# Kernel tuning notes

Hardware: AMD Instinct MI355X
Metric: run time of the kernel (lower is better)

Reference implementation:

```python
import jax, jax.numpy as jnp
import numpy as np

N = 50000      # num_nodes
NT = 300000    # unique (s, o) pairs
R = 64         # num relations
RP = 16        # latent pseudo-relations
E = 32         # emb_dim
C = 32         # num_classes
LW = 64        # latent MLP width


def setup_inputs() -> dict:
    key = jax.random.key(0)
    ks = jax.random.split(key, 12)
    inp = {
        "s_idx": jax.random.randint(ks[0], (NT,), 0, N, dtype=jnp.int32),
        "o_idx": jax.random.randint(ks[1], (NT,), 0, N, dtype=jnp.int32),
        "nhots": jax.random.uniform(ks[2], (NT, R), dtype=jnp.float32),
        "W1a": jax.random.normal(ks[3], (R, LW), dtype=jnp.float32) * 0.1,
        "b1a": jnp.zeros((LW,), jnp.float32),
        "W1b": jax.random.normal(ks[4], (LW, RP), dtype=jnp.float32) * 0.1,
        "b1b": jnp.zeros((RP,), jnp.float32),
        "W2a": jax.random.normal(ks[5], (R, LW), dtype=jnp.float32) * 0.1,
        "b2a": jnp.zeros((LW,), jnp.float32),
        "W2b": jax.random.normal(ks[6], (LW, RP), dtype=jnp.float32) * 0.1,
        "b2b": jnp.zeros((RP,), jnp.float32),
        "weights1": jax.random.normal(ks[7], (RP, N, E), dtype=jnp.float32) * 0.05,
        "weights2": jax.random.normal(ks[8], (RP, E, C), dtype=jnp.float32) * 0.05,
        "bias1": jnp.zeros((E,), jnp.float32),
        "bias2": jnp.zeros((C,), jnp.float32),
    }
    return inp


def _mlp(x, Wa, ba, Wb, bb):
    # Linear(r, lwidth) -> ReLU -> Linear(lwidth, rp)
    return jax.nn.relu(x @ Wa + ba) @ Wb + bb


def reference(s_idx, o_idx, nhots, W1a, b1a, W1b, b1b, W2a, b2a, W2b, b2b,
              weights1, weights2, bias1, bias2):
    n, rp = N, RP
    e = weights1.shape[2]
    k = jnp.arange(rp, dtype=s_idx.dtype)[:, None]   # [rp, 1]

    # hindices: rows = s (tiled k-major), cols = o * k  -> sparse (n, n*rp)
    hrows = jnp.tile(s_idx, rp)                       # [rp*nt]
    hcols = (o_idx[None, :] * k).reshape(-1)          # [rp*nt]
    # vindices: rows = s * k, cols = o (tiled)        -> sparse (n*rp, n)
    vrows = (s_idx[None, :] * k).reshape(-1)
    vcols = jnp.tile(o_idx, rp)

    # ---- layer 1: latent relation softmax + column-normalized spmm ----
    lat1 = jax.nn.softmax(_mlp(nhots, W1a, b1a, W1b, b1b), axis=1)  # [nt, rp]
    v1 = lat1.T.reshape(-1)                                          # [rp*nt], k-major
    colsum = jax.ops.segment_sum(v1, hcols, num_segments=n * rp)
    v1 = v1 / colsum[hcols]
    # spmm: out[s] += v1 * weights1.view(rp*n, e)[o*k]
    h = jax.ops.segment_sum(v1[:, None] * weights1.reshape(rp * n, e)[hcols],
                            hrows, num_segments=n)                   # [n, e]
    h = jax.nn.relu(h + bias1)

    # ---- layer 2: latent relation softmax + row-normalized spmm ----
    lat2 = jax.nn.softmax(_mlp(nhots, W2a, b2a, W2b, b2b), axis=1)   # [nt, rp]
    v2 = lat2.T.reshape(-1)
    rowsum = jax.ops.segment_sum(v2, vrows, num_segments=n * rp)
    v2 = v2 / rowsum[vrows]
    # spmm: out[s*k] += v2 * h[o]
    h2 = jax.ops.segment_sum(v2[:, None] * h[vcols],
                             vrows, num_segments=n * rp)             # [n*rp, e]
    h2 = h2.reshape(rp, n, e)

    out = jnp.einsum('rhc,rnh->nc', weights2, h2) + bias2            # [n, c]
    return out
```

## Files before the change

### kernel.cpp

```cpp
#include <hip/hip_runtime.h>
#include <hip/hip_bf16.h>

#define DEV_INLINE __device__ __forceinline__

constexpr int kN   = 50000;
constexpr int kNT  = 300000;
constexpr int kR   = 64;
constexpr int kRP  = 16;
constexpr int kE   = 32;
constexpr int kC   = 32;
constexpr int kLW  = 64;
constexpr int kNRP = kN * kRP;
constexpr int kChunks = (kN + 255) / 256;

typedef __attribute__((ext_vector_type(8))) short s8v;
typedef __attribute__((ext_vector_type(4))) float f32x4;

DEV_INLINE short f2bf(float f) {
  union { float f; unsigned u; } v; v.f = f;
  unsigned r = (v.u + 0x7fffu + ((v.u >> 16) & 1u)) >> 16;
  return (short)r;
}
DEV_INLINE float bf2f(short s) {
  union { unsigned u; float f; } v; v.u = ((unsigned)(unsigned short)s) << 16;
  return v.f;
}
DEV_INLINE float bflo(unsigned u) { union { unsigned x; float f; } a; a.x = u << 16;        return a.f; }
DEV_INLINE float bfhi(unsigned u) { union { unsigned x; float f; } a; a.x = u & 0xffff0000u; return a.f; }

union U4S8 { uint4 u; s8v s; };

DEV_INLINE void split8(const float4 A, const float4 B, s8v& hi, s8v& lo) {
  const float f[8] = {A.x, A.y, A.z, A.w, B.x, B.y, B.z, B.w};
  unsigned u[8], l[8];
#pragma unroll
  for (int i = 0; i < 8; i++) { union { float f; unsigned u; } c; c.f = f[i]; u[i] = c.u; }
#pragma unroll
  for (int i = 0; i < 8; i++) {
    union { unsigned u; float f; } t; t.u = u[i] & 0xffff0000u;
    union { float f; unsigned u; } c; c.f = f[i] - t.f; l[i] = c.u;
  }
  U4S8 H, L;
  H.u.x = (u[1] & 0xffff0000u) | (u[0] >> 16);
  H.u.y = (u[3] & 0xffff0000u) | (u[2] >> 16);
  H.u.z = (u[5] & 0xffff0000u) | (u[4] >> 16);
  H.u.w = (u[7] & 0xffff0000u) | (u[6] >> 16);
  L.u.x = (l[1] & 0xffff0000u) | (l[0] >> 16);
  L.u.y = (l[3] & 0xffff0000u) | (l[2] >> 16);
  L.u.z = (l[5] & 0xffff0000u) | (l[4] >> 16);
  L.u.w = (l[7] & 0xffff0000u) | (l[6] >> 16);
  hi = H.s; lo = L.s;
}

__global__ void __launch_bounds__(256)
k_count(const int* __restrict__ s_idx, const int* __restrict__ o_idx,
        int* __restrict__ cnt_s, int* __restrict__ cnt_o) {
  const int e = blockIdx.x * 256 + threadIdx.x;
  if (e < kNT) {
    atomicAdd(&cnt_s[s_idx[e]], 1);
    atomicAdd(&cnt_o[o_idx[e]], 1);
  }
}

__global__ void __launch_bounds__(256)
k_scan_p1(const int* __restrict__ cnt_s, const int* __restrict__ cnt_o,
          int* __restrict__ rp_s, int* __restrict__ rp_o,
          int* __restrict__ bs_s, int* __restrict__ bs_o) {
  const int b = blockIdx.x;
  const bool iso = b >= kChunks;
  const int chunk = iso ? b - kChunks : b;
  const int* cnt = iso ? cnt_o : cnt_s;
  int* rp = iso ? rp_o : rp_s;
  int* bs = iso ? bs_o : bs_s;
  __shared__ int ws[4];
  const int tid = threadIdx.x, wave = tid >> 6, lane = tid & 63;
  const int i = chunk * 256 + tid;
  int v = (i < kN) ? cnt[i] : 0;
  int incl = v;
#pragma unroll
  for (int off = 1; off < 64; off <<= 1) {
    int tmp = __shfl_up(incl, off, 64);
    if (lane >= off) incl += tmp;
  }
  if (lane == 63) ws[wave] = incl;
  __syncthreads();
  int add = 0;
#pragma unroll
  for (int w = 0; w < 4; w++) if (w < wave) add += ws[w];
  incl += add;
  if (i < kN) rp[i + 1] = incl;
  if (tid == 255) bs[chunk] = incl;
}

__global__ void __launch_bounds__(256)
k_scan_p2(int* __restrict__ bs_s, int* __restrict__ bs_o) {
  __shared__ int ws[4];
  const int tid = threadIdx.x, wave = tid >> 6, lane = tid & 63;
#pragma unroll 1
  for (int a = 0; a < 2; a++) {
    int* bs = a ? bs_o : bs_s;
    const int v = (tid < kChunks) ? bs[tid] : 0;
    int incl = v;
#pragma unroll
    for (int off = 1; off < 64; off <<= 1) {
      int tmp = __shfl_up(incl, off, 64);
      if (lane >= off) incl += tmp;
    }
    if (lane == 63) ws[wave] = incl;
    __syncthreads();
    int add = 0;
#pragma unroll
    for (int w = 0; w < 4; w++) if (w < wave) add += ws[w];
    incl += add;
    __syncthreads();
    if (tid < kChunks) bs[tid] = incl - v;
    __syncthreads();
  }
}

__global__ void __launch_bounds__(256)
k_scan_p3(const int* __restrict__ bs_s, const int* __restrict__ bs_o,
          int* __restrict__ rp_s, int* __restrict__ rp_o) {
  const int b = blockIdx.x;
  const bool iso = b >= kChunks;
  const int chunk = iso ? b - kChunks : b;
  int* rp = iso ? rp_o : rp_s;
  const int* bs = iso ? bs_o : bs_s;
  const int i = chunk * 256 + threadIdx.x;
  if (i < kN) rp[i + 1] += bs[chunk];
  if (chunk == 0 && threadIdx.x == 0) rp[0] = 0;
}

__global__ void __launch_bounds__(256)
k_scatter2(const int* __restrict__ s_idx, const int* __restrict__ o_idx,
           const int* __restrict__ rowptr_s, int* __restrict__ cursor_s,
           const int* __restrict__ rowptr_o, int* __restrict__ cursor_o,
           int2* __restrict__ eo_s, int* __restrict__ e_o) {
  const int e = blockIdx.x * 256 + threadIdx.x;
  if (e < kNT) {
    const int s = s_idx[e], o = o_idx[e];
    const int ps = atomicAdd(&cursor_s[s], 1);
    int2 v; v.x = e; v.y = o;
    eo_s[rowptr_s[s] + ps] = v;
    const int po = atomicAdd(&cursor_o[o], 1);
    e_o[rowptr_o[o] + po] = e;
  }
}

__global__ void __launch_bounds__(256)
k_wprep(const float* __restrict__ W1a, const float* __restrict__ W1b,
        const float* __restrict__ W2a, const float* __restrict__ W2b,
        short* __restrict__ Wf) {
  const int tid = threadIdx.x;
  for (int i = tid; i < 8192; i += 256) {
    const int j = i & 7, lane = (i >> 3) & 63, ks = (i >> 9) & 1,
              nt = (i >> 10) & 3, mlp = i >> 12;
    const int p = lane & 15, q8 = (lane >> 4) * 8;
    const float* Wa = mlp ? W2a : W1a;
    const float v = Wa[(ks * 32 + q8 + j) * kLW + nt * 16 + p];
    union { float f; unsigned u; } c; c.f = v;
    const short h = (short)(c.u >> 16);
    Wf[i] = h;
    Wf[8192 + i] = f2bf(v - bf2f(h));
  }
  for (int i = tid; i < 2048; i += 256) {
    const int j = i & 7, lane = (i >> 3) & 63, ks = (i >> 9) & 1, mlp = i >> 10;
    const int p = lane & 15, q8 = (lane >> 4) * 8;
    const float* Wb = mlp ? W2b : W1b;
    const float v = Wb[(ks * 32 + q8 + j) * kRP + p];
    union { float f; unsigned u; } c; c.f = v;
    const short h = (short)(c.u >> 16);
    Wf[16384 + i] = h;
    Wf[18432 + i] = f2bf(v - bf2f(h));
  }
}

__global__ void __launch_bounds__(256)
k_lat(const float* __restrict__ nhots, const short* __restrict__ Wf,
      const float* __restrict__ b1a, const float* __restrict__ b1b,
      const float* __restrict__ b2a, const float* __restrict__ b2b,
      float* __restrict__ lat1o, float* __restrict__ lat2o) {
  __shared__ float sHf[4][16][68];
  const int tid = threadIdx.x;
  const int wave = tid >> 6, lane = tid & 63;
  const int p = lane & 15, q = lane >> 4, q8 = (lane >> 4) * 8;

  const uint4* BaH4 = (const uint4*)(Wf);
  const uint4* BaL4 = (const uint4*)(Wf + 8192);
  const uint4* BbH4 = (const uint4*)(Wf + 16384);
  const uint4* BbL4 = (const uint4*)(Wf + 18432);

  const int w2 = (blockIdx.x * 4 + wave) * 2;

#pragma unroll 1
  for (int mlp = 0; mlp < 2; mlp++) {
    s8v Bh[4][2], Bl[4][2], Bbh[2], Bbl[2];
#pragma unroll
    for (int nt = 0; nt < 4; nt++)
#pragma unroll
      for (int ks = 0; ks < 2; ks++) {
        U4S8 a, b;
        a.u = BaH4[((mlp * 4 + nt) * 2 + ks) * 64 + lane];
        b.u = BaL4[((mlp * 4 + nt) * 2 + ks) * 64 + lane];
        Bh[nt][ks] = a.s; Bl[nt][ks] = b.s;
      }
#pragma unroll
    for (int ks = 0; ks < 2; ks++) {
      U4S8 a, b;
      a.u = BbH4[(mlp * 2 + ks) * 64 + lane];
      b.u = BbL4[(mlp * 2 + ks) * 64 + lane];
      Bbh[ks] = a.s; Bbl[ks] = b.s;
    }
    const float* bA = mlp ? b2a : b1a;
    const float* bB = mlp ? b2b : b1b;
    float bav[4];
#pragma unroll
    for (int nt = 0; nt < 4; nt++) bav[nt] = bA[nt * 16 + p];
    const float bbv = bB[p];
    float* lato = mlp ? lat2o : lat1o;

#pragma unroll 1
    for (int t = 0; t < 2; t++) {
      const int slot = w2 + t;
      if (slot >= kNT / 32) break;
      const int eb = slot * 32;
#pragma unroll 1
      for (int ht = 0; ht < 2; ht++) {
        const int mb = eb + ht * 16;
        const float* arow = nhots + (size_t)(mb + p) * kR;
        s8v ah[2], al[2];
#pragma unroll
        for (int ks = 0; ks < 2; ks++) {
          const float4 xa = *(const float4*)(arow + ks * 32 + q8);
          const float4 xb = *(const float4*)(arow + ks * 32 + q8 + 4);
          split8(xa, xb, ah[ks], al[ks]);
        }
        f32x4 acc[4];
#pragma unroll
        for (int nt = 0; nt < 4; nt++) {
          acc[nt] = (f32x4)0.f;
#pragma unroll
          for (int ks = 0; ks < 2; ks++) {
            acc[nt] = __builtin_amdgcn_mfma_f32_16x16x32_bf16(ah[ks], Bh[nt][ks], acc[nt], 0, 0, 0);
            acc[nt] = __builtin_amdgcn_mfma_f32_16x16x32_bf16(ah[ks], Bl[nt][ks], acc[nt], 0, 0, 0);
            acc[nt] = __builtin_amdgcn_mfma_f32_16x16x32_bf16(al[ks], Bh[nt][ks], acc[nt], 0, 0, 0);
          }
        }
#pragma unroll
        for (int nt = 0; nt < 4; nt++)
#pragma unroll
          for (int reg = 0; reg < 4; reg++)
            sHf[wave][q * 4 + reg][nt * 16 + p] = fmaxf(acc[nt][reg] + bav[nt], 0.f);
        const float* hr = &sHf[wave][p][0];
        s8v hh[2], hl[2];
#pragma unroll
        for (int ks = 0; ks < 2; ks++) {
          const float4 xa = *(const float4*)(hr + ks * 32 + q8);
          const float4 xb = *(const float4*)(hr + ks * 32 + q8 + 4);
          split8(xa, xb, hh[ks], hl[ks]);
        }
        f32x4 accB = (f32x4)0.f;
#pragma unroll
        for (int ks = 0; ks < 2; ks++) {
          accB = __builtin_amdgcn_mfma_f32_16x16x32_bf16(hh[ks], Bbh[ks], accB, 0, 0, 0);
          accB = __builtin_amdgcn_mfma_f32_16x16x32_bf16(hh[ks], Bbl[ks], accB, 0, 0, 0);
          accB = __builtin_amdgcn_mfma_f32_16x16x32_bf16(hl[ks], Bbh[ks], accB, 0, 0, 0);
        }
#pragma unroll
        for (int reg = 0; reg < 4; reg++) {
          const float v = accB[reg] + bbv;
          float m = v;
#pragma unroll
          for (int d = 1; d < 16; d <<= 1) m = fmaxf(m, __shfl_xor(m, d));
          const float e = __expf(v - m);
          float sum = e;
#pragma unroll
          for (int d = 1; d < 16; d <<= 1) sum += __shfl_xor(sum, d);
          lato[(size_t)(mb + q * 4 + reg) * kRP + p] = e / sum;
        }
      }
    }
  }
}

__global__ void __launch_bounds__(256)
k_partials(const int* __restrict__ rowptr_s, const int2* __restrict__ eo_s,
           const int* __restrict__ rowptr_o, const int* __restrict__ e_o,
           const float* __restrict__ lat1, const float* __restrict__ lat2,
           float* __restrict__ C1, float* __restrict__ R2,
           float* __restrict__ tots) {
  __shared__ float st[2][4];
  const int tid = threadIdx.x;
  const int wave = tid >> 6, lane = tid & 63;
  const int k = lane & 15, g = lane >> 4;
  float t1 = 0.f, t2 = 0.f;
  const int nw = gridDim.x * 4;
  for (int n = blockIdx.x * 4 + wave; n < kN; n += nw) {
    {
      const int beg = rowptr_s[n], end = rowptr_s[n + 1];
      float acc = 0.f;
      for (int j = beg + g; j < end; j += 4)
        acc += lat2[(size_t)eo_s[j].x * kRP + k];
      acc += __shfl_xor(acc, 16); acc += __shfl_xor(acc, 32);
      if (g == 0) { R2[n * kRP + k] = acc; if (k == 0) t2 += acc; }
    }
    {
      const int beg = rowptr_o[n], end = rowptr_o[n + 1];
      float acc = 0.f;
      for (int j = beg + g; j < end; j += 4)
        acc += lat1[(size_t)e_o[j] * kRP + k];
      acc += __shfl_xor(acc, 16); acc += __shfl_xor(acc, 32);
      if (g == 0) { C1[n * kRP + k] = acc; if (k == 0) t1 += acc; }
    }
  }
  if (lane == 0) { st[0][wave] = t1; st[1][wave] = t2; }
  __syncthreads();
  if (tid == 0) {
    atomicAdd(&tots[0], st[0][0] + st[0][1] + st[0][2] + st[0][3]);
    atomicAdd(&tots[1], st[1][0] + st[1][1] + st[1][2] + st[1][3]);
  }
}

__global__ void __launch_bounds__(256)
k_norms(const float* __restrict__ C1, const float* __restrict__ R2,
        const float* __restrict__ tots,
        float* __restrict__ csinv, float* __restrict__ rsinv) {
  const int m = blockIdx.x * 256 + threadIdx.x;
  if (m < kNRP) {
    float cs = (m == 0) ? tots[0] : 0.f;
    float rs = (m == 0) ? tots[1] : 0.f;
#pragma unroll
    for (int k = 1; k < kRP; k++) {
      if (m % k == 0) {
        const int q = m / k;
        if (q < kN) { cs += C1[q * kRP + k]; rs += R2[q * kRP + k]; }
      }
    }
    csinv[m] = (cs != 0.f) ? 1.f / cs : 0.f;
    rsinv[m] = (rs != 0.f) ? 1.f / rs : 0.f;
  }
}

__global__ void __launch_bounds__(256)
k_gbuild(const float* __restrict__ wt1, const float* __restrict__ csinv,
         unsigned* __restrict__ G8u) {
  __shared__ float sT[16][33];
  const int o = blockIdx.x;
  const int tid = threadIdx.x;
#pragma unroll
  for (int half = 0; half < 2; half++) {
    const int e = half * 256 + tid;
    const int k = e >> 5, c = e & 31;
    const int idx = o * k;
    sT[k][c] = csinv[idx] * wt1[(size_t)idx * kE + c];
  }
  __syncthreads();
  const int l = tid >> 2;
  const int c = l >> 1, kh = l & 1;
  const int j0 = (2 * tid) & 7;
  const int k0 = kh * 8 + j0, k1 = k0 + 1;
  const unsigned lo = (unsigned short)f2bf(sT[k0][c]);
  const unsigned hi = (unsigned short)f2bf(sT[k1][c]);
  G8u[(size_t)o * 256 + tid] = lo | (hi << 16);
}

__global__ void __launch_bounds__(256)
k_layer1g(const int* __restrict__ rowptr, const int2* __restrict__ eo,
          const float* __restrict__ lat1, const uint4* __restrict__ G8,
          const float* __restrict__ bias1, float* __restrict__ h) {
  const int tid = threadIdx.x;
  const int wave = tid >> 6, lane = tid & 63;
  const int c = lane >> 1, kh = lane & 1;
  const float b1 = bias1[c];
  for (int s = blockIdx.x * 4 + wave; s < kN; s += gridDim.x * 4) {
    float acc = 0.f;
    const int beg = rowptr[s], end = rowptr[s + 1];
    for (int j = beg; j < end; j++) {
      const int2 E = eo[j];
      const uint4 g = G8[(size_t)E.y * 64 + lane];
      const float4 la = *(const float4*)(lat1 + (size_t)E.x * kRP + kh * 8);
      const float4 lb = *(const float4*)(lat1 + (size_t)E.x * kRP + kh * 8 + 4);
      acc = fmaf(la.x, bflo(g.x), acc); acc = fmaf(la.y, bfhi(g.x), acc);
      acc = fmaf(la.z, bflo(g.y), acc); acc = fmaf(la.w, bfhi(g.y), acc);
      acc = fmaf(lb.x, bflo(g.z), acc); acc = fmaf(lb.y, bfhi(g.z), acc);
      acc = fmaf(lb.z, bflo(g.w), acc); acc = fmaf(lb.w, bfhi(g.w), acc);
    }
    acc += __shfl_xor(acc, 1);
    if (kh == 0) h[(size_t)s * kE + c] = fmaxf(acc + b1, 0.f);
  }
}

__global__ void __launch_bounds__(256)
k_u(const int* __restrict__ rowptr, const int2* __restrict__ eo,
    const float* __restrict__ lat2, const float* __restrict__ rsinv,
    const float* __restrict__ h, short* __restrict__ Ub,
    float* __restrict__ pblk) {
  __shared__ float sacc[kE];
  const int tid = threadIdx.x;
  const int wave = tid >> 6, lane = tid & 63;
  const int c = lane & 31, half = lane >> 5;
  if (tid < kE) sacc[tid] = 0.f;
  __syncthreads();
  float hpart = 0.f;
  for (int s = blockIdx.x * 4 + wave; s < kN; s += gridDim.x * 4) {
    float u[8];
#pragma unroll
    for (int kk = 0; kk < 8; kk++) u[kk] = 0.f;
    const int beg = rowptr[s], end = rowptr[s + 1];
    for (int j = beg; j < end; j++) {
      const int2 E = eo[j];
      const float hv = h[(size_t)E.y * kE + c];
      const float4* lp = (const float4*)(lat2 + (size_t)E.x * kRP) + half * 2;
      const float4 la = lp[0], lb = lp[1];
      const float lv[8] = {la.x, la.y, la.z, la.w, lb.x, lb.y, lb.z, lb.w};
#pragma unroll
      for (int kk = 0; kk < 8; kk++) u[kk] = fmaf(lv[kk], hv, u[kk]);
    }
    if (half == 0) hpart += u[0];
#pragma unroll
    for (int kk = 0; kk < 8; kk++) {
      const int k = half * 8 + kk;
      if (k >= 1)
        Ub[((size_t)s * 15 + (k - 1)) * kE + c] = f2bf(u[kk] * rsinv[s * k]);
    }
  }
  atomicAdd(&sacc[c], hpart);
  __syncthreads();
  if (tid < kE) pblk[(size_t)blockIdx.x * kE + tid] = sacc[tid];
}

__global__ void __launch_bounds__(256)
k_hred(const float* __restrict__ pblk, int nblk, float* __restrict__ hrow0) {
  __shared__ float sacc[kE];
  const int tid = threadIdx.x;
  if (tid < kE) sacc[tid] = 0.f;
  __syncthreads();
  const int total = nblk * kE;
  float r = 0.f;
  for (int i = blockIdx.x * 256 + tid; i < total; i += gridDim.x * 256)
    r += pblk[i];
  atomicAdd(&sacc[tid & 31], r);
  __syncthreads();
  if (tid < kE) atomicAdd(&hrow0[tid], sacc[tid]);
}

__global__ void __launch_bounds__(256)
k_h2(const short* __restrict__ Ub, const float* __restrict__ hrow0,
     const float* __restrict__ rsinv, short* __restrict__ H2) {
  const int tid = threadIdx.x;
  const int g = tid >> 5, c = tid & 31;
  const int n = blockIdx.x * 8 + g;
  const float rs0 = rsinv[0];
  int nm[16];
  nm[0] = 0; nm[1] = 0;
#pragma unroll
  for (int k = 2; k < kRP; k++) nm[k] = n % k;
#pragma unroll
  for (int r = 0; r < kRP; r++) {
    float row = 0.f;
    if (r == 0 && n == 0) row = hrow0[c] * rs0;
#pragma unroll
    for (int k = r + 1; k < kRP; k++) {
      const int target = (k - (r * 50000) % k) % k;
      if (nm[k] == target) {
        const int s = (r * 50000 + n) / k;
        row += bf2f(Ub[((size_t)s * 15 + (k - 1)) * kE + c]);
      }
    }
    H2[((size_t)n * kRP + r) * kE + c] = f2bf(row);
  }
}

__global__ void __launch_bounds__(256)
k_einsum(const short* __restrict__ H2, const float* __restrict__ W2,
         const float* __restrict__ bias2, float* __restrict__ out) {
  __shared__ short sBWh[16 * 2 * 64 * 8];
  __shared__ short sBWl[16 * 2 * 64 * 8];
  const int tid = threadIdx.x;
  for (int i = tid; i < 16384; i += 256) {
    const int j = i & 7, ln = (i >> 3) & 63, nt = (i >> 9) & 1, ks = i >> 10;
    const int pp = ln & 15, qq8 = (ln >> 4) * 8;
    const float v = W2[(ks * 32 + qq8 + j) * 32 + nt * 16 + pp];
    const short h = f2bf(v);
    sBWh[i] = h;
    sBWl[i] = f2bf(v - bf2f(h));
  }
  __syncthreads();
  const int wave = tid >> 6, lane = tid & 63;
  const int p = lane & 15, q = lane >> 4, q8 = q * 8;
  const float bias0 = bias2[p], bias1v = bias2[16 + p];
  for (int tile = blockIdx.x * 4 + wave; tile < kN / 16; tile += gridDim.x * 4) {
    const int mb = tile * 16;
    f32x4 acc0 = (f32x4)0.f, acc1 = (f32x4)0.f;
    const short* arow = H2 + (size_t)(mb + p) * 512 + q8;
#pragma unroll
    for (int ks = 0; ks < 16; ks++) {
      const s8v a   = *(const s8v*)(arow + ks * 32);
      const s8v b0h = *(const s8v*)(sBWh + ((ks * 2 + 0) * 64 + lane) * 8);
      const s8v b0l = *(const s8v*)(sBWl + ((ks * 2 + 0) * 64 + lane) * 8);
      const s8v b1h = *(const s8v*)(sBWh + ((ks * 2 + 1) * 64 + lane) * 8);
      const s8v b1l = *(const s8v*)(sBWl + ((ks * 2 + 1) * 64 + lane) * 8);
      acc0 = __builtin_amdgcn_mfma_f32_16x16x32_bf16(a, b0h, acc0, 0, 0, 0);
      acc0 = __builtin_amdgcn_mfma_f32_16x16x32_bf16(a, b0l, acc0, 0, 0, 0);
      acc1 = __builtin_amdgcn_mfma_f32_16x16x32_bf16(a, b1h, acc1, 0, 0, 0);
      acc1 = __builtin_amdgcn_mfma_f32_16x16x32_bf16(a, b1l, acc1, 0, 0, 0);
    }
#pragma unroll
    for (int reg = 0; reg < 4; reg++) {
      const int n = mb + q * 4 + reg;
      out[(size_t)n * kC + p]      = acc0[reg] + bias0;
      out[(size_t)n * kC + 16 + p] = acc1[reg] + bias1v;
    }
  }
}

extern "C" void kernel_launch(void* const* d_in, const int* in_sizes, int n_in,
                              void* d_out, int out_size, void* d_ws, size_t ws_size,
                              hipStream_t stream) {
  (void)in_sizes; (void)n_in; (void)out_size; (void)ws_size;
  const int* s_idx = (const int*)d_in[0];
  const int* o_idx = (const int*)d_in[1];
  const float* nhots = (const float*)d_in[2];
  const float* W1a = (const float*)d_in[3]; const float* b1a = (const float*)d_in[4];
  const float* W1b = (const float*)d_in[5]; const float* b1b = (const float*)d_in[6];
  const float* W2a = (const float*)d_in[7]; const float* b2a = (const float*)d_in[8];
  const float* W2b = (const float*)d_in[9]; const float* b2b = (const float*)d_in[10];
  const float* wt1 = (const float*)d_in[11]; const float* wt2 = (const float*)d_in[12];
  const float* bias1 = (const float*)d_in[13]; const float* bias2 = (const float*)d_in[14];

  char* ws = (char*)d_ws;
  size_t off = 0;
  auto alloc = [&](size_t bytes) -> char* {
    char* p = ws + off;
    off = (off + bytes + 255) & ~(size_t)255;
    return p;
  };
  char*  z0       = ws;
  int*   cnt_s    = (int*)  alloc((size_t)kN * 4);
  int*   cnt_o    = (int*)  alloc((size_t)kN * 4);
  int*   cursor_s = (int*)  alloc((size_t)kN * 4);
  int*   cursor_o = (int*)  alloc((size_t)kN * 4);
  float* tots     = (float*)alloc(8);
  float* hrow0    = (float*)alloc((size_t)kE * 4);
  const size_t zbytes = (size_t)((ws + off) - z0);
  short* Wf       = (short*)alloc((size_t)20480 * 2);
  int*   bs_s     = (int*)  alloc((size_t)kChunks * 4);
  int*   bs_o     = (int*)  alloc((size_t)kChunks * 4);
  int*   rowptr_s = (int*)  alloc((size_t)(kN + 1) * 4);
  int*   rowptr_o = (int*)  alloc((size_t)(kN + 1) * 4);
  float* pblk     = (float*)alloc((size_t)12500 * kE * 4);
  float* lat2     = (float*)alloc((size_t)kNT * kRP * 4);
  int2*  eo_s     = (int2*) alloc((size_t)kNT * 8);
  int*   e_o      = (int*)  alloc((size_t)kNT * 4);
  float* C1       = (float*)alloc((size_t)kNRP * 4);
  float* R2       = (float*)alloc((size_t)kNRP * 4);
  float* csinv    = (float*)alloc((size_t)kNRP * 4);
  float* rsinv    = (float*)alloc((size_t)kNRP * 4);
  float* hbuf     = (float*)alloc((size_t)kN * kE * 4);
  short* Ub       = (short*)alloc((size_t)kN * 15 * kE * 2);
  char*  Greg     = alloc((size_t)kN * 1024);
  float* lat1     = (float*)Ub;
  unsigned* G8u   = (unsigned*)Greg;
  short* H2       = (short*)Greg;

  hipMemsetAsync(z0, 0, zbytes, stream);

  const dim3 blk(256);
  const int gEdges = (kNT + 255) / 256;
  const int gLat = ((kNT / 32 + 1) / 2 + 3) / 4;

  k_count<<<gEdges, blk, 0, stream>>>(s_idx, o_idx, cnt_s, cnt_o);
  k_scan_p1<<<2 * kChunks, blk, 0, stream>>>(cnt_s, cnt_o, rowptr_s, rowptr_o, bs_s, bs_o);
  k_scan_p2<<<1, blk, 0, stream>>>(bs_s, bs_o);
  k_scan_p3<<<2 * kChunks, blk, 0, stream>>>(bs_s, bs_o, rowptr_s, rowptr_o);
  k_scatter2<<<gEdges, blk, 0, stream>>>(s_idx, o_idx, rowptr_s, cursor_s,
                                         rowptr_o, cursor_o, eo_s, e_o);
  k_wprep<<<1, blk, 0, stream>>>(W1a, W1b, W2a, W2b, Wf);
  k_lat<<<gLat, blk, 0, stream>>>(nhots, Wf, b1a, b1b, b2a, b2b, lat1, lat2);
  k_partials<<<512, blk, 0, stream>>>(rowptr_s, eo_s, rowptr_o, e_o,
                                      lat1, lat2, C1, R2, tots);
  k_norms<<<(kNRP + 255) / 256, blk, 0, stream>>>(C1, R2, tots, csinv, rsinv);
  k_gbuild<<<kN, blk, 0, stream>>>(wt1, csinv, G8u);
  k_layer1g<<<12500, blk, 0, stream>>>(rowptr_s, eo_s, lat1, (const uint4*)G8u, bias1, hbuf);
  k_u<<<12500, blk, 0, stream>>>(rowptr_s, eo_s, lat2, rsinv, hbuf, Ub, pblk);
  k_hred<<<50, blk, 0, stream>>>(pblk, 12500, hrow0);
  k_h2<<<kN / 8, blk, 0, stream>>>(Ub, hrow0, rsinv, H2);
  k_einsum<<<782, blk, 0, stream>>>(H2, wt2, bias2, (float*)d_out);
}
```

Measured before the change: 642.9 us.

## Fuse H2 construction into einsum kernel and precompute W2 split in wprep

Removes the separate k_h2 kernel that materialized the bf16 H2 buffer (N*16*32) and builds each MFMA A-fragment on the fly from Ub gathers inside the einsum kernel. The hi/lo bf16 split of weights2 moves into a second block of k_wprep, so each einsum block copies it from global memory instead of recomputing it. k_partials' grid also grows from 512 to 6250 blocks. This saves a global write and read of H2 and one launch, at the cost of scattered, less coalesced Ub loads inside the MFMA loop.

Result: slower. 805.6 us (+25.3%).

```diff
diff --git a/kernel.cpp b/kernel.cpp
--- a/kernel.cpp
+++ b/kernel.cpp
@@ -150,28 +150,39 @@
 __global__ void __launch_bounds__(256)
 k_wprep(const float* __restrict__ W1a, const float* __restrict__ W1b,
         const float* __restrict__ W2a, const float* __restrict__ W2b,
-        short* __restrict__ Wf) {
-  const int tid = threadIdx.x;
-  for (int i = tid; i < 8192; i += 256) {
-    const int j = i & 7, lane = (i >> 3) & 63, ks = (i >> 9) & 1,
-              nt = (i >> 10) & 3, mlp = i >> 12;
-    const int p = lane & 15, q8 = (lane >> 4) * 8;
-    const float* Wa = mlp ? W2a : W1a;
-    const float v = Wa[(ks * 32 + q8 + j) * kLW + nt * 16 + p];
-    union { float f; unsigned u; } c; c.f = v;
-    const short h = (short)(c.u >> 16);
-    Wf[i] = h;
-    Wf[8192 + i] = f2bf(v - bf2f(h));
-  }
-  for (int i = tid; i < 2048; i += 256) {
-    const int j = i & 7, lane = (i >> 3) & 63, ks = (i >> 9) & 1, mlp = i >> 10;
-    const int p = lane & 15, q8 = (lane >> 4) * 8;
-    const float* Wb = mlp ? W2b : W1b;
-    const float v = Wb[(ks * 32 + q8 + j) * kRP + p];
-    union { float f; unsigned u; } c; c.f = v;
-    const short h = (short)(c.u >> 16);
-    Wf[16384 + i] = h;
-    Wf[18432 + i] = f2bf(v - bf2f(h));
+        const float* __restrict__ W2, short* __restrict__ Wf) {
+  const int tid = threadIdx.x;
+  if (blockIdx.x == 0) {
+    for (int i = tid; i < 8192; i += 256) {
+      const int j = i & 7, lane = (i >> 3) & 63, ks = (i >> 9) & 1,
+                nt = (i >> 10) & 3, mlp = i >> 12;
+      const int p = lane & 15, q8 = (lane >> 4) * 8;
+      const float* Wa = mlp ? W2a : W1a;
+      const float v = Wa[(ks * 32 + q8 + j) * kLW + nt * 16 + p];
+      union { float f; unsigned u; } c; c.f = v;
+      const short h = (short)(c.u >> 16);
+      Wf[i] = h;
+      Wf[8192 + i] = f2bf(v - bf2f(h));
+    }
+    for (int i = tid; i < 2048; i += 256) {
+      const int j = i & 7, lane = (i >> 3) & 63, ks = (i >> 9) & 1, mlp = i >> 10;
+      const int p = lane & 15, q8 = (lane >> 4) * 8;
+      const float* Wb = mlp ? W2b : W1b;
+      const float v = Wb[(ks * 32 + q8 + j) * kRP + p];
+      union { float f; unsigned u; } c; c.f = v;
+      const short h = (short)(c.u >> 16);
+      Wf[16384 + i] = h;
+      Wf[18432 + i] = f2bf(v - bf2f(h));
+    }
+  } else {
+    for (int i = tid; i < 16384; i += 256) {
+      const int j = i & 7, ln = (i >> 3) & 63, nt = (i >> 9) & 1, ks = i >> 10;
+      const int pp = ln & 15, qq8 = (ln >> 4) * 8;
+      const float v = W2[(ks * 32 + qq8 + j) * 32 + nt * 16 + pp];
+      const short h = f2bf(v);
+      Wf[20480 + i] = h;
+      Wf[36864 + i] = f2bf(v - bf2f(h));
+    }
   }
 }
 
@@ -445,57 +456,62 @@
 }
 
 __global__ void __launch_bounds__(256)
-k_h2(const short* __restrict__ Ub, const float* __restrict__ hrow0,
-     const float* __restrict__ rsinv, short* __restrict__ H2) {
-  const int tid = threadIdx.x;
-  const int g = tid >> 5, c = tid & 31;
-  const int n = blockIdx.x * 8 + g;
-  const float rs0 = rsinv[0];
-  int nm[16];
-  nm[0] = 0; nm[1] = 0;
-#pragma unroll
-  for (int k = 2; k < kRP; k++) nm[k] = n % k;
-#pragma unroll
-  for (int r = 0; r < kRP; r++) {
-    float row = 0.f;
-    if (r == 0 && n == 0) row = hrow0[c] * rs0;
-#pragma unroll
-    for (int k = r + 1; k < kRP; k++) {
-      const int target = (k - (r * 50000) % k) % k;
-      if (nm[k] == target) {
-        const int s = (r * 50000 + n) / k;
-        row += bf2f(Ub[((size_t)s * 15 + (k - 1)) * kE + c]);
-      }
-    }
-    H2[((size_t)n * kRP + r) * kE + c] = f2bf(row);
-  }
-}
-
-__global__ void __launch_bounds__(256)
-k_einsum(const short* __restrict__ H2, const float* __restrict__ W2,
-         const float* __restrict__ bias2, float* __restrict__ out) {
-  __shared__ short sBWh[16 * 2 * 64 * 8];
-  __shared__ short sBWl[16 * 2 * 64 * 8];
-  const int tid = threadIdx.x;
-  for (int i = tid; i < 16384; i += 256) {
-    const int j = i & 7, ln = (i >> 3) & 63, nt = (i >> 9) & 1, ks = i >> 10;
-    const int pp = ln & 15, qq8 = (ln >> 4) * 8;
-    const float v = W2[(ks * 32 + qq8 + j) * 32 + nt * 16 + pp];
-    const short h = f2bf(v);
-    sBWh[i] = h;
-    sBWl[i] = f2bf(v - bf2f(h));
+k_einsum_fused(const short* __restrict__ Ub, const float* __restrict__ hrow0,
+               const float* __restrict__ rsinv, const short* __restrict__ Wf,
+               const float* __restrict__ bias2, float* __restrict__ out) {
+  __shared__ short sBWh[16384];
+  __shared__ short sBWl[16384];
+  const int tid = threadIdx.x;
+  {
+    const uint4* src_h = (const uint4*)(Wf + 20480);
+    const uint4* src_l = (const uint4*)(Wf + 36864);
+    uint4* dh = (uint4*)sBWh;
+    uint4* dl = (uint4*)sBWl;
+    for (int i = tid; i < 2048; i += 256) { dh[i] = src_h[i]; dl[i] = src_l[i]; }
   }
   __syncthreads();
   const int wave = tid >> 6, lane = tid & 63;
   const int p = lane & 15, q = lane >> 4, q8 = q * 8;
   const float bias0 = bias2[p], bias1v = bias2[16 + p];
+  const float rs0 = rsinv[0];
   for (int tile = blockIdx.x * 4 + wave; tile < kN / 16; tile += gridDim.x * 4) {
     const int mb = tile * 16;
+    const int n = mb + p;
+    int nm[kRP];
+#pragma unroll
+    for (int k = 2; k < kRP; k++) nm[k] = n % k;
     f32x4 acc0 = (f32x4)0.f, acc1 = (f32x4)0.f;
-    const short* arow = H2 + (size_t)(mb + p) * 512 + q8;
 #pragma unroll
     for (int ks = 0; ks < 16; ks++) {
-      const s8v a   = *(const s8v*)(arow + ks * 32);
+      float row[8];
+#pragma unroll
+      for (int i = 0; i < 8; i++) row[i] = 0.f;
+      if (ks == 0) {
+        const uint4 g = *(const uint4*)(Ub + (size_t)n * 15 * kE + q8);
+        row[0] += bflo(g.x); row[1] += bfhi(g.x);
+        row[2] += bflo(g.y); row[3] += bfhi(g.y);
+        row[4] += bflo(g.z); row[5] += bfhi(g.z);
+        row[6] += bflo(g.w); row[7] += bfhi(g.w);
+        if (n == 0) {
+#pragma unroll
+          for (int i = 0; i < 8; i++) row[i] += hrow0[q8 + i] * rs0;
+        }
+      }
+#pragma unroll
+      for (int k = (ks == 0 ? 2 : ks + 1); k < kRP; k++) {
+        const int target = (k - (ks * 50000) % k) % k;
+        if (nm[k] == target) {
+          const int s = (ks * 50000 + n) / k;
+          const uint4 g = *(const uint4*)(Ub + ((size_t)s * 15 + (k - 1)) * kE + q8);
+          row[0] += bflo(g.x); row[1] += bfhi(g.x);
+          row[2] += bflo(g.y); row[3] += bfhi(g.y);
+          row[4] += bflo(g.z); row[5] += bfhi(g.z);
+          row[6] += bflo(g.w); row[7] += bfhi(g.w);
+        }
+      }
+      s8v a;
+#pragma unroll
+      for (int i = 0; i < 8; i++) a[i] = f2bf(row[i]);
       const s8v b0h = *(const s8v*)(sBWh + ((ks * 2 + 0) * 64 + lane) * 8);
       const s8v b0l = *(const s8v*)(sBWl + ((ks * 2 + 0) * 64 + lane) * 8);
       const s8v b1h = *(const s8v*)(sBWh + ((ks * 2 + 1) * 64 + lane) * 8);
@@ -507,9 +523,9 @@
     }
 #pragma unroll
     for (int reg = 0; reg < 4; reg++) {
-      const int n = mb + q * 4 + reg;
-      out[(size_t)n * kC + p]      = acc0[reg] + bias0;
-      out[(size_t)n * kC + 16 + p] = acc1[reg] + bias1v;
+      const int nn = mb + q * 4 + reg;
+      out[(size_t)nn * kC + p]      = acc0[reg] + bias0;
+      out[(size_t)nn * kC + 16 + p] = acc1[reg] + bias1v;
     }
   }
 }
@@ -543,7 +559,7 @@
   float* tots     = (float*)alloc(8);
   float* hrow0    = (float*)alloc((size_t)kE * 4);
   const size_t zbytes = (size_t)((ws + off) - z0);
-  short* Wf       = (short*)alloc((size_t)20480 * 2);
+  short* Wf       = (short*)alloc((size_t)53248 * 2);
   int*   bs_s     = (int*)  alloc((size_t)kChunks * 4);
   int*   bs_o     = (int*)  alloc((size_t)kChunks * 4);
   int*   rowptr_s = (int*)  alloc((size_t)(kN + 1) * 4);
@@ -561,7 +577,6 @@
   char*  Greg     = alloc((size_t)kN * 1024);
   float* lat1     = (float*)Ub;
   unsigned* G8u   = (unsigned*)Greg;
-  short* H2       = (short*)Greg;
 
   hipMemsetAsync(z0, 0, zbytes, stream);
 
@@ -575,15 +590,14 @@
   k_scan_p3<<<2 * kChunks, blk, 0, stream>>>(bs_s, bs_o, rowptr_s, rowptr_o);
   k_scatter2<<<gEdges, blk, 0, stream>>>(s_idx, o_idx, rowptr_s, cursor_s,
                                          rowptr_o, cursor_o, eo_s, e_o);
-  k_wprep<<<1, blk, 0, stream>>>(W1a, W1b, W2a, W2b, Wf);
+  k_wprep<<<2, blk, 0, stream>>>(W1a, W1b, W2a, W2b, wt2, Wf);
   k_lat<<<gLat, blk, 0, stream>>>(nhots, Wf, b1a, b1b, b2a, b2b, lat1, lat2);
-  k_partials<<<512, blk, 0, stream>>>(rowptr_s, eo_s, rowptr_o, e_o,
-                                      lat1, lat2, C1, R2, tots);
+  k_partials<<<6250, blk, 0, stream>>>(rowptr_s, eo_s, rowptr_o, e_o,
+                                       lat1, lat2, C1, R2, tots);
   k_norms<<<(kNRP + 255) / 256, blk, 0, stream>>>(C1, R2, tots, csinv, rsinv);
   k_gbuild<<<kN, blk, 0, stream>>>(wt1, csinv, G8u);
   k_layer1g<<<12500, blk, 0, stream>>>(rowptr_s, eo_s, lat1, (const uint4*)G8u, bias1, hbuf);
   k_u<<<12500, blk, 0, stream>>>(rowptr_s, eo_s, lat2, rsinv, hbuf, Ub, pblk);
   k_hred<<<50, blk, 0, stream>>>(pblk, 12500, hrow0);
-  k_h2<<<kN / 8, blk, 0, stream>>>(Ub, hrow0, rsinv, H2);
-  k_einsum<<<782, blk, 0, stream>>>(H2, wt2, bias2, (float*)d_out);
-}
+  k_einsum_fused<<<782, blk, 0, stream>>>(Ub, hrow0, rsinv, Wf, bias2, (float*)d_out);
+}
```
